# Kernel tuning notes

Hardware: AMD Instinct MI355X
Metric: run time of the kernel (lower is better)

The kernel has to match this reference:

```python
import jax, jax.numpy as jnp
import numpy as np

B, O, H2, L, S = 256, 1024, 2048, 2, 12  # batch, output_dim, 2*hidden_dim, num_layers, enc seq len


def setup_inputs() -> dict:
    key = jax.random.key(0)
    ks = jax.random.split(key, 18)
    def rn(k, shape, scale=1.0):
        return jax.random.normal(k, shape, jnp.float32) * scale
    s = 0.02  # weight scale to keep softmax/gates in a sane range
    return {
        "x": rn(ks[0], (1, B, O)),
        "h0": rn(ks[1], (L, B, H2)),
        "c0": rn(ks[2], (L, B, H2)),
        "encoder_outputs": rn(ks[3], (S, B, H2)),
        "attn_W": rn(ks[4], (S, H2 + O), s), "attn_b": rn(ks[5], (S,), s),
        "comb_W": rn(ks[6], (O, H2 + O), s), "comb_b": rn(ks[7], (O,), s),
        "Wih0": rn(ks[8], (4 * H2, O), s), "Whh0": rn(ks[9], (4 * H2, H2), s),
        "bih0": rn(ks[10], (4 * H2,), s), "bhh0": rn(ks[11], (4 * H2,), s),
        "Wih1": rn(ks[12], (4 * H2, H2), s), "Whh1": rn(ks[13], (4 * H2, H2), s),
        "bih1": rn(ks[14], (4 * H2,), s), "bhh1": rn(ks[15], (4 * H2,), s),
        "out_W": rn(ks[16], (O, H2), s), "out_b": rn(ks[17], (O,), s),
    }


def _lstm_cell(x, h, c, Wih, Whh, bih, bhh):
    # PyTorch LSTM cell: gates in (i, f, g, o) order
    gates = x @ Wih.T + bih + h @ Whh.T + bhh  # [B, 4*H2]
    i, f, g, o = jnp.split(gates, 4, axis=-1)
    c_new = jax.nn.sigmoid(f) * c + jax.nn.sigmoid(i) * jnp.tanh(g)
    h_new = jax.nn.sigmoid(o) * jnp.tanh(c_new)
    return h_new, c_new


def reference(x, h0, c0, encoder_outputs, attn_W, attn_b, comb_W, comb_b,
              Wih0, Whh0, bih0, bhh0, Wih1, Whh1, bih1, bhh1, out_W, out_b):
    x0 = x[0]  # [B, O]
    # Bahdanau-style attention over the 12 encoder steps
    attn_in = jnp.concatenate([x0, h0[0]], axis=1)               # [B, O+2H]
    attn_weights = jax.nn.softmax(attn_in @ attn_W.T + attn_b, axis=1)  # [B, S]
    attn_applied = jnp.einsum('bs,sbh->bh', attn_weights, encoder_outputs)  # [B, 2H]
    # combine + relu
    xc = jnp.concatenate([x0, attn_applied], axis=1)             # [B, O+2H]
    xin = jax.nn.relu(xc @ comb_W.T + comb_b)                    # [B, O]
    # single-step 2-layer LSTM (dropout=0)
    h1, c1 = _lstm_cell(xin, h0[0], c0[0], Wih0, Whh0, bih0, bhh0)
    h2, c2 = _lstm_cell(h1, h0[1], c0[1], Wih1, Whh1, bih1, bhh1)
    output = h2[None]                                            # [1, B, 2H]
    prediction = output @ out_W.T + out_b                        # [1, B, O]
    h_new = jnp.stack([h1, h2], axis=0)
    c_new = jnp.stack([c1, c2], axis=0)
    return prediction, h_new, c_new
```

## Files before the change

### kernel.cpp

```cpp
#include <hip/hip_runtime.h>
#include <hip/hip_bf16.h>

typedef short short8 __attribute__((ext_vector_type(8)));
typedef short short4v __attribute__((ext_vector_type(4)));
typedef float floatx4 __attribute__((ext_vector_type(4)));

#define BB 256
#define OO 1024
#define HH 2048
#define SS 12
#define LSTRIDE 72

__device__ __forceinline__ __hip_bfloat16 f2b(float x) { return __float2bfloat16(x); }
__device__ __forceinline__ float sigf(float x) { return 1.0f / (1.0f + expf(-x)); }

__device__ __forceinline__ short8 cvt8v(float4 lo, float4 hi) {
    union { short8 s; __hip_bfloat16 h[8]; } u;
    u.h[0] = f2b(lo.x); u.h[1] = f2b(lo.y); u.h[2] = f2b(lo.z); u.h[3] = f2b(lo.w);
    u.h[4] = f2b(hi.x); u.h[5] = f2b(hi.y); u.h[6] = f2b(hi.z); u.h[7] = f2b(hi.w);
    return u.s;
}
__device__ __forceinline__ short4v cvt4v(float4 v) {
    union { short4v s; __hip_bfloat16 h[4]; } u;
    u.h[0] = f2b(v.x); u.h[1] = f2b(v.y); u.h[2] = f2b(v.z); u.h[3] = f2b(v.w);
    return u.s;
}

__global__ __launch_bounds__(256)
void attn_logits(const float* __restrict__ x0,
                 const float* __restrict__ h00,
                 const float* __restrict__ attn_W,
                 const float* __restrict__ attn_b,
                 float* __restrict__ wts)
{
    const int b = blockIdx.x;
    const int tid = threadIdx.x;
    const int lane = tid & 63;
    const int wave = tid >> 6;

    float part[SS];
#pragma unroll
    for (int s = 0; s < SS; s++) part[s] = 0.f;

#pragma unroll
    for (int k = 0; k < 3; k++) {
        const int c = tid + (k << 8);
        float4 v = (k == 0) ? *(const float4*)(x0 + (size_t)b * OO + (c << 2))
                            : *(const float4*)(h00 + (size_t)b * HH + ((c - 256) << 2));
#pragma unroll
        for (int s = 0; s < SS; s++) {
            float4 w4 = *(const float4*)(attn_W + (size_t)s * (OO + HH) + (c << 2));
            part[s] += v.x * w4.x + v.y * w4.y + v.z * w4.z + v.w * w4.w;
        }
    }
#pragma unroll
    for (int s = 0; s < SS; s++) {
#pragma unroll
        for (int off = 32; off > 0; off >>= 1)
            part[s] += __shfl_down(part[s], off);
    }
    __shared__ float red[4][SS];
    if (lane == 0) {
#pragma unroll
        for (int s = 0; s < SS; s++) red[wave][s] = part[s];
    }
    __syncthreads();
    if (tid == 0) {
        float logits[SS];
        float mx = -1e30f;
        for (int s = 0; s < SS; s++) {
            logits[s] = red[0][s] + red[1][s] + red[2][s] + red[3][s] + attn_b[s];
            mx = fmaxf(mx, logits[s]);
        }
        float sum = 0.f;
        for (int s = 0; s < SS; s++) { logits[s] = expf(logits[s] - mx); sum += logits[s]; }
        float inv = 1.0f / sum;
        for (int s = 0; s < SS; s++) wts[b * SS + s] = logits[s] * inv;
    }
}

__global__ __launch_bounds__(256)
void attn_apply(const float* __restrict__ enc,
                const float* __restrict__ wts,
                float* __restrict__ attn_out)
{
    const int b = blockIdx.x >> 1;
    const int half = blockIdx.x & 1;
    const int tid = threadIdx.x;
    __shared__ float w[SS];
    if (tid < SS) w[tid] = wts[b * SS + tid];
    __syncthreads();
    const int h = (half << 10) + (tid << 2);
    float4 a = {0.f, 0.f, 0.f, 0.f};
#pragma unroll
    for (int s = 0; s < SS; s++) {
        float4 e = *(const float4*)(enc + ((size_t)(s * BB + b) * HH) + h);
        float ws = w[s];
        a.x += ws * e.x; a.y += ws * e.y; a.z += ws * e.z; a.w += ws * e.w;
    }
    *(float4*)(attn_out + (size_t)b * HH + h) = a;
}

template<int K1, int K2, bool RELU>
__global__ __launch_bounds__(256)
void gemm_dual(const float* __restrict__ A1,
               const float* __restrict__ W1, int ldw1, int ofs1,
               const float* __restrict__ A2,
               const float* __restrict__ W2, int ldw2, int ofs2,
               const float* __restrict__ bias1,
               const float* __restrict__ bias2,
               float* __restrict__ Cout, int ldc)
{
    constexpr int n1 = K1 >> 6;
    constexpr int nT = (K1 + K2) >> 6;
    __shared__ __attribute__((aligned(16))) __hip_bfloat16 As[2][16][LSTRIDE];
    __shared__ __attribute__((aligned(16))) __hip_bfloat16 Ws[2][32][LSTRIDE];
    __shared__ float red[2][16][17];
    const int tid = threadIdx.x;
    const int lane = tid & 63;
    const int wave = tid >> 6;
    const int quad = lane >> 4, l15 = lane & 15;
    const int cf = wave & 1;
    const int kh = wave >> 1;
    const int m_base = blockIdx.y * 16;
    const int n_base = blockIdx.x * 32;

    const int arow = tid >> 4, acol = (tid & 15) << 2;
    const int wrow = tid >> 3, wcol = (tid & 7) << 3;

    const float* baseA1 = A1 + (size_t)(m_base + arow) * K1 + acol;
    const float* baseA2 = A2 + (size_t)(m_base + arow) * K2 + acol;
    const float* baseW1 = W1 + (size_t)(n_base + wrow) * ldw1 + ofs1 + wcol;
    const float* baseW2 = W2 + (size_t)(n_base + wrow) * ldw2 + ofs2 + wcol;

    float4 pa, pw0, pw1;
    auto issue = [&](int tt) {
        const float *ap, *wp;
        if (tt < n1) { ap = baseA1 + (tt << 6);        wp = baseW1 + (tt << 6); }
        else         { ap = baseA2 + ((tt - n1) << 6); wp = baseW2 + ((tt - n1) << 6); }
        pa  = *(const float4*)(ap);
        pw0 = *(const float4*)(wp);
        pw1 = *(const float4*)(wp + 4);
    };
    issue(0);

    floatx4 acc = (floatx4){0.f, 0.f, 0.f, 0.f};
    for (int t = 0; t < nT; t++) {
        const int buf = t & 1;
        *(short4v*)(&As[buf][arow][acol]) = cvt4v(pa);
        *(short8*)(&Ws[buf][wrow][wcol])  = cvt8v(pw0, pw1);
        __syncthreads();
        if (t + 1 < nT) issue(t + 1);
        short8 af = *(const short8*)(&As[buf][l15][kh * 32 + quad * 8]);
        short8 bf = *(const short8*)(&Ws[buf][cf * 16 + l15][kh * 32 + quad * 8]);
        acc = __builtin_amdgcn_mfma_f32_16x16x32_bf16(af, bf, acc, 0, 0, 0);
    }

    if (kh == 1) {
#pragma unroll
        for (int r = 0; r < 4; r++) red[cf][l15][quad * 4 + r] = acc[r];
    }
    __syncthreads();
    if (kh == 0) {
        const int col = n_base + cf * 16 + l15;
        float bsum = bias1[col] + (bias2 ? bias2[col] : 0.f);
#pragma unroll
        for (int r = 0; r < 4; r++) {
            const int row = m_base + quad * 4 + r;
            float v = acc[r] + red[cf][l15][quad * 4 + r] + bsum;
            if (RELU) v = fmaxf(v, 0.f);
            Cout[(size_t)row * ldc + col] = v;
        }
    }
}

template<int K1>
__global__ __launch_bounds__(512)
void lstm_fused(const float* __restrict__ A1,
                const float* __restrict__ Wih,
                const float* __restrict__ A2,
                const float* __restrict__ Whh,
                const float* __restrict__ bih,
                const float* __restrict__ bhh,
                const float* __restrict__ c0,
                float* __restrict__ h_out,
                float* __restrict__ c_out)
{
    constexpr int n1 = K1 >> 6;
    constexpr int nT = n1 + (HH >> 6);
    __shared__ __attribute__((aligned(16))) __hip_bfloat16 As[2][128][LSTRIDE];
    __shared__ __attribute__((aligned(16))) __hip_bfloat16 Ws[2][64][LSTRIDE];
    const int tid = threadIdx.x;
    const int lane = tid & 63;
    const int wave = tid >> 6;
    const int quad = lane >> 4, l15 = lane & 15;

    const int L    = blockIdx.x + (blockIdx.y << 7);
    const int xcd  = L & 7;
    const int slot = L >> 3;
    const int by   = xcd >> 2;
    const int bx   = ((xcd & 3) << 5) + slot;
    const int m_base = by * 128;
    const int n_base = bx * 16;

    const int arow = tid >> 2, acol = (tid & 3) << 4;
    const int wrow = tid >> 3, wcol = (tid & 7) << 3;
    const int grow = (wrow >> 4) * HH + n_base + (wrow & 15);

    const float* baseA1 = A1 + (size_t)(m_base + arow) * K1 + acol;
    const float* baseA2 = A2 + (size_t)(m_base + arow) * HH + acol;
    const float* baseW1 = Wih + (size_t)grow * K1 + wcol;
    const float* baseW2 = Whh + (size_t)grow * HH + wcol;

    float4 paA[4], pwA[2], paB[4], pwB[2];
    auto issue = [&](int tt, float4 (&pa)[4], float4 (&pw)[2]) {
        const float *ap, *wp;
        if (tt < n1) { ap = baseA1 + (tt << 6);        wp = baseW1 + (tt << 6); }
        else         { ap = baseA2 + ((tt - n1) << 6); wp = baseW2 + ((tt - n1) << 6); }
#pragma unroll
        for (int j = 0; j < 4; j++) pa[j] = *(const float4*)(ap + (j << 2));
#pragma unroll
        for (int j = 0; j < 2; j++) pw[j] = *(const float4*)(wp + (j << 2));
    };
    issue(0, paA, pwA);
    issue(1, paB, pwB);

    floatx4 acc[4];
#pragma unroll
    for (int g = 0; g < 4; g++) acc[g] = (floatx4){0.f, 0.f, 0.f, 0.f};

    auto compute = [&](int buf) {
#pragma unroll
        for (int k = 0; k < 2; k++) {
            short8 af = *(const short8*)(&As[buf][wave * 16 + l15][k * 32 + quad * 8]);
#pragma unroll
            for (int g = 0; g < 4; g++) {
                short8 bf = *(const short8*)(&Ws[buf][g * 16 + l15][k * 32 + quad * 8]);
                acc[g] = __builtin_amdgcn_mfma_f32_16x16x32_bf16(af, bf, acc[g], 0, 0, 0);
            }
        }
    };

    for (int t = 0; t < nT; t += 2) {
        *(short8*)(&As[0][arow][acol])     = cvt8v(paA[0], paA[1]);
        *(short8*)(&As[0][arow][acol + 8]) = cvt8v(paA[2], paA[3]);
        *(short8*)(&Ws[0][wrow][wcol])     = cvt8v(pwA[0], pwA[1]);
        if (t + 2 < nT) issue(t + 2, paA, pwA);
        __syncthreads();
        compute(0);
        *(short8*)(&As[1][arow][acol])     = cvt8v(paB[0], paB[1]);
        *(short8*)(&As[1][arow][acol + 8]) = cvt8v(paB[2], paB[3]);
        *(short8*)(&Ws[1][wrow][wcol])     = cvt8v(pwB[0], pwB[1]);
        if (t + 3 < nT) issue(t + 3, paB, pwB);
        __syncthreads();
        compute(1);
    }

    const int col = n_base + l15;
    float bsum[4];
#pragma unroll
    for (int g = 0; g < 4; g++)
        bsum[g] = bih[g * HH + col] + bhh[g * HH + col];

#pragma unroll
    for (int r = 0; r < 4; r++) {
        const int row = m_base + wave * 16 + quad * 4 + r;
        const size_t idx = (size_t)row * HH + col;
        float gi = acc[0][r] + bsum[0];
        float gf = acc[1][r] + bsum[1];
        float gg = acc[2][r] + bsum[2];
        float go = acc[3][r] + bsum[3];
        float c0v = c0[idx];
        float cn = sigf(gf) * c0v + sigf(gi) * tanhf(gg);
        float hn = sigf(go) * tanhf(cn);
        h_out[idx] = hn;
        c_out[idx] = cn;
    }
}

extern "C" void kernel_launch(void* const* d_in, const int* in_sizes, int n_in,
                              void* d_out, int out_size, void* d_ws, size_t ws_size,
                              hipStream_t stream) {
    const float* x      = (const float*)d_in[0];
    const float* h0     = (const float*)d_in[1];
    const float* c0     = (const float*)d_in[2];
    const float* enc    = (const float*)d_in[3];
    const float* attn_W = (const float*)d_in[4];
    const float* attn_b = (const float*)d_in[5];
    const float* comb_W = (const float*)d_in[6];
    const float* comb_b = (const float*)d_in[7];
    const float* Wih0   = (const float*)d_in[8];
    const float* Whh0   = (const float*)d_in[9];
    const float* bih0   = (const float*)d_in[10];
    const float* bhh0   = (const float*)d_in[11];
    const float* Wih1   = (const float*)d_in[12];
    const float* Whh1   = (const float*)d_in[13];
    const float* bih1   = (const float*)d_in[14];
    const float* bhh1   = (const float*)d_in[15];
    const float* out_W  = (const float*)d_in[16];
    const float* out_b  = (const float*)d_in[17];

    float* pred = (float*)d_out;
    float* h1   = pred + 262144;
    float* h2   = h1 + 524288;
    float* c1   = h2 + 524288;
    float* c2   = c1 + 524288;
    const float* h0_l0 = h0;
    const float* h0_l1 = h0 + 524288;
    const float* c0_l0 = c0;
    const float* c0_l1 = c0 + 524288;

    float* xin      = pred;
    float* attn_out = c2;
    float* wts      = c1;

    attn_logits<<<dim3(BB), dim3(256), 0, stream>>>(x, h0_l0, attn_W, attn_b, wts);

    attn_apply<<<dim3(BB * 2), dim3(256), 0, stream>>>(enc, wts, attn_out);

    gemm_dual<OO, HH, true><<<dim3(OO / 32, BB / 16), dim3(256), 0, stream>>>(
        x, comb_W, OO + HH, 0,
        attn_out, comb_W, OO + HH, OO,
        comb_b, nullptr, xin, OO);

    lstm_fused<OO><<<dim3(HH / 16, BB / 128), dim3(512), 0, stream>>>(
        xin, Wih0, h0_l0, Whh0, bih0, bhh0, c0_l0, h1, c1);

    lstm_fused<HH><<<dim3(HH / 16, BB / 128), dim3(512), 0, stream>>>(
        h1, Wih1, h0_l1, Whh1, bih1, bhh1, c0_l1, h2, c2);

    gemm_dual<HH, 0, false><<<dim3(OO / 32, BB / 16), dim3(256), 0, stream>>>(
        h2, out_W, HH, 0,
        h2, out_W, HH, 0,
        out_b, nullptr, pred, OO);
}
```

Measured before the change: 404.7 us.

## Split LSTM gate GEMM into split-K tiles with swizzled LDS and separate cell kernel

Replaces the fused LSTM kernel with a split-K gate GEMM: each block covers all 256 batch rows and 32 columns per gate, with K split four ways, and writes fp32 partial gate sums to workspace. A separate elementwise kernel adds the partials and biases, then applies the LSTM cell. Larger tiles reuse each weight load across the whole batch instead of reloading it for two row halves, and XOR-swizzled LDS replaces padded rows to avoid bank conflicts. The cost is an extra launch per layer and roughly 32MB of partial-sum traffic per layer through workspace.

```diff
diff --git a/kernel.cpp b/kernel.cpp
--- a/kernel.cpp
+++ b/kernel.cpp
@@ -174,49 +174,58 @@
     }
 }
 
+#define A_BUF_BYTES 16384
+#define W_BUF_BYTES 8192
+__device__ __forceinline__ int swzA(int buf, int row, int c8) {
+    return (buf << 14) + ((((row << 6) | (c8 << 4))) ^ ((row & 7) << 4));
+}
+__device__ __forceinline__ int swzW(int buf, int row, int c8) {
+    return 2 * A_BUF_BYTES + (buf << 13) + ((((row << 6) | (c8 << 4))) ^ ((row & 7) << 4));
+}
+
 template<int K1>
 __global__ __launch_bounds__(512)
-void lstm_fused(const float* __restrict__ A1,
+void lstm_gates(const float* __restrict__ A1,
                 const float* __restrict__ Wih,
                 const float* __restrict__ A2,
                 const float* __restrict__ Whh,
-                const float* __restrict__ bih,
-                const float* __restrict__ bhh,
-                const float* __restrict__ c0,
-                float* __restrict__ h_out,
-                float* __restrict__ c_out)
-{
-    constexpr int n1 = K1 >> 6;
-    constexpr int nT = n1 + (HH >> 6);
-    __shared__ __attribute__((aligned(16))) __hip_bfloat16 As[2][128][LSTRIDE];
-    __shared__ __attribute__((aligned(16))) __hip_bfloat16 Ws[2][64][LSTRIDE];
+                float* __restrict__ P)
+{
+    constexpr int KTOT = K1 + HH;
+    constexpr int KPER = KTOT / 4;
+    constexpr int NT = KPER / 32;
+    __shared__ __attribute__((aligned(128))) unsigned char lds[2 * A_BUF_BYTES + 2 * W_BUF_BYTES];
+
     const int tid = threadIdx.x;
     const int lane = tid & 63;
     const int wave = tid >> 6;
     const int quad = lane >> 4, l15 = lane & 15;
 
-    const int L    = blockIdx.x + (blockIdx.y << 7);
+    const int L    = blockIdx.x + (blockIdx.y << 6);
     const int xcd  = L & 7;
     const int slot = L >> 3;
-    const int by   = xcd >> 2;
-    const int bx   = ((xcd & 3) << 5) + slot;
-    const int m_base = by * 128;
-    const int n_base = bx * 16;
-
-    const int arow = tid >> 2, acol = (tid & 3) << 4;
-    const int wrow = tid >> 3, wcol = (tid & 7) << 3;
-    const int grow = (wrow >> 4) * HH + n_base + (wrow & 15);
-
-    const float* baseA1 = A1 + (size_t)(m_base + arow) * K1 + acol;
-    const float* baseA2 = A2 + (size_t)(m_base + arow) * HH + acol;
-    const float* baseW1 = Wih + (size_t)grow * K1 + wcol;
-    const float* baseW2 = Whh + (size_t)grow * HH + wcol;
+    const int ks   = xcd >> 1;
+    const int nb   = ((xcd & 1) << 5) | slot;
+    const int n_base = nb << 5;
+    const int k0 = ks * KPER;
+
+    const int arow = tid >> 1;
+    const int ac8  = (tid & 1) << 1;
+    const int wrow = tid >> 2;
+    const int wc8  = tid & 3;
+    const int grow = (wrow >> 5) * HH + n_base + (wrow & 31);
+
+    const float* bA1 = A1 + (size_t)arow * K1 + (ac8 << 3);
+    const float* bA2 = A2 + (size_t)arow * HH + (ac8 << 3);
+    const float* bW1 = Wih + (size_t)grow * K1 + (wc8 << 3);
+    const float* bW2 = Whh + (size_t)grow * HH + (wc8 << 3);
 
     float4 paA[4], pwA[2], paB[4], pwB[2];
     auto issue = [&](int tt, float4 (&pa)[4], float4 (&pw)[2]) {
+        const int gk = k0 + (tt << 5);
         const float *ap, *wp;
-        if (tt < n1) { ap = baseA1 + (tt << 6);        wp = baseW1 + (tt << 6); }
-        else         { ap = baseA2 + ((tt - n1) << 6); wp = baseW2 + ((tt - n1) << 6); }
+        if (gk < K1) { ap = bA1 + gk;        wp = bW1 + gk; }
+        else         { ap = bA2 + (gk - K1); wp = bW2 + (gk - K1); }
 #pragma unroll
         for (int j = 0; j < 4; j++) pa[j] = *(const float4*)(ap + (j << 2));
 #pragma unroll
@@ -225,57 +234,104 @@
     issue(0, paA, pwA);
     issue(1, paB, pwB);
 
-    floatx4 acc[4];
-#pragma unroll
-    for (int g = 0; g < 4; g++) acc[g] = (floatx4){0.f, 0.f, 0.f, 0.f};
-
+    floatx4 acc[2][4][2];
+#pragma unroll
+    for (int mf = 0; mf < 2; mf++)
+#pragma unroll
+        for (int g = 0; g < 4; g++)
+#pragma unroll
+            for (int nf = 0; nf < 2; nf++)
+                acc[mf][g][nf] = (floatx4){0.f, 0.f, 0.f, 0.f};
+
+    auto store_tile = [&](int buf, float4 (&pa)[4], float4 (&pw)[2]) {
+        *(short8*)(lds + swzA(buf, arow, ac8))     = cvt8v(pa[0], pa[1]);
+        *(short8*)(lds + swzA(buf, arow, ac8 | 1)) = cvt8v(pa[2], pa[3]);
+        *(short8*)(lds + swzW(buf, wrow, wc8))     = cvt8v(pw[0], pw[1]);
+    };
     auto compute = [&](int buf) {
-#pragma unroll
-        for (int k = 0; k < 2; k++) {
-            short8 af = *(const short8*)(&As[buf][wave * 16 + l15][k * 32 + quad * 8]);
-#pragma unroll
-            for (int g = 0; g < 4; g++) {
-                short8 bf = *(const short8*)(&Ws[buf][g * 16 + l15][k * 32 + quad * 8]);
-                acc[g] = __builtin_amdgcn_mfma_f32_16x16x32_bf16(af, bf, acc[g], 0, 0, 0);
+        short8 af[2];
+#pragma unroll
+        for (int mf = 0; mf < 2; mf++)
+            af[mf] = *(const short8*)(lds + swzA(buf, (wave << 5) + (mf << 4) + l15, quad));
+#pragma unroll
+        for (int g = 0; g < 4; g++)
+#pragma unroll
+            for (int nf = 0; nf < 2; nf++) {
+                short8 bf = *(const short8*)(lds + swzW(buf, (g << 5) + (nf << 4) + l15, quad));
+                acc[0][g][nf] = __builtin_amdgcn_mfma_f32_16x16x32_bf16(af[0], bf, acc[0][g][nf], 0, 0, 0);
+                acc[1][g][nf] = __builtin_amdgcn_mfma_f32_16x16x32_bf16(af[1], bf, acc[1][g][nf], 0, 0, 0);
             }
-        }
     };
 
-    for (int t = 0; t < nT; t += 2) {
-        *(short8*)(&As[0][arow][acol])     = cvt8v(paA[0], paA[1]);
-        *(short8*)(&As[0][arow][acol + 8]) = cvt8v(paA[2], paA[3]);
-        *(short8*)(&Ws[0][wrow][wcol])     = cvt8v(pwA[0], pwA[1]);
-        if (t + 2 < nT) issue(t + 2, paA, pwA);
+    for (int t = 0; t < NT; t += 2) {
+        store_tile(0, paA, pwA);
+        if (t + 2 < NT) issue(t + 2, paA, pwA);
         __syncthreads();
         compute(0);
-        *(short8*)(&As[1][arow][acol])     = cvt8v(paB[0], paB[1]);
-        *(short8*)(&As[1][arow][acol + 8]) = cvt8v(paB[2], paB[3]);
-        *(short8*)(&Ws[1][wrow][wcol])     = cvt8v(pwB[0], pwB[1]);
-        if (t + 3 < nT) issue(t + 3, paB, pwB);
+        store_tile(1, paB, pwB);
+        if (t + 3 < NT) issue(t + 3, paB, pwB);
         __syncthreads();
         compute(1);
     }
 
-    const int col = n_base + l15;
-    float bsum[4];
-#pragma unroll
-    for (int g = 0; g < 4; g++)
-        bsum[g] = bih[g * HH + col] + bhh[g * HH + col];
-
-#pragma unroll
-    for (int r = 0; r < 4; r++) {
-        const int row = m_base + wave * 16 + quad * 4 + r;
-        const size_t idx = (size_t)row * HH + col;
-        float gi = acc[0][r] + bsum[0];
-        float gf = acc[1][r] + bsum[1];
-        float gg = acc[2][r] + bsum[2];
-        float go = acc[3][r] + bsum[3];
-        float c0v = c0[idx];
-        float cn = sigf(gf) * c0v + sigf(gi) * tanhf(gg);
-        float hn = sigf(go) * tanhf(cn);
-        h_out[idx] = hn;
-        c_out[idx] = cn;
-    }
+    float* Pk = P + (size_t)ks * (256 * 8192);
+#pragma unroll
+    for (int mf = 0; mf < 2; mf++)
+#pragma unroll
+        for (int g = 0; g < 4; g++)
+#pragma unroll
+            for (int nf = 0; nf < 2; nf++) {
+                const int col = n_base + (nf << 4) + l15;
+#pragma unroll
+                for (int r = 0; r < 4; r++) {
+                    const int row = (wave << 5) + (mf << 4) + (quad << 2) + r;
+                    Pk[(size_t)row * 8192 + g * HH + col] = acc[mf][g][nf][r];
+                }
+            }
+}
+
+__global__ __launch_bounds__(512)
+void lstm_cell(const float* __restrict__ P,
+               const float* __restrict__ bih,
+               const float* __restrict__ bhh,
+               const float* __restrict__ c0,
+               float* __restrict__ h_out,
+               float* __restrict__ c_out)
+{
+    const int gid = blockIdx.x * 512 + threadIdx.x;
+    const int row = gid >> 9;
+    const int col = (gid & 511) << 2;
+
+    float4 gate[4];
+#pragma unroll
+    for (int g = 0; g < 4; g++) {
+        const size_t base = (size_t)row * 8192 + g * HH + col;
+        float4 s = *(const float4*)(P + base);
+#pragma unroll
+        for (int k = 1; k < 4; k++) {
+            float4 v = *(const float4*)(P + (size_t)k * (256 * 8192) + base);
+            s.x += v.x; s.y += v.y; s.z += v.z; s.w += v.w;
+        }
+        float4 b1 = *(const float4*)(bih + g * HH + col);
+        float4 b2 = *(const float4*)(bhh + g * HH + col);
+        s.x += b1.x + b2.x; s.y += b1.y + b2.y; s.z += b1.z + b2.z; s.w += b1.w + b2.w;
+        gate[g] = s;
+    }
+    const size_t idx = (size_t)row * HH + col;
+    float4 cv = *(const float4*)(c0 + idx);
+    float4 hn, cn;
+    {
+        float c_ = sigf(gate[1].x) * cv.x + sigf(gate[0].x) * tanhf(gate[2].x);
+        cn.x = c_; hn.x = sigf(gate[3].x) * tanhf(c_);
+        c_ = sigf(gate[1].y) * cv.y + sigf(gate[0].y) * tanhf(gate[2].y);
+        cn.y = c_; hn.y = sigf(gate[3].y) * tanhf(c_);
+        c_ = sigf(gate[1].z) * cv.z + sigf(gate[0].z) * tanhf(gate[2].z);
+        cn.z = c_; hn.z = sigf(gate[3].z) * tanhf(c_);
+        c_ = sigf(gate[1].w) * cv.w + sigf(gate[0].w) * tanhf(gate[2].w);
+        cn.w = c_; hn.w = sigf(gate[3].w) * tanhf(c_);
+    }
+    *(float4*)(h_out + idx) = hn;
+    *(float4*)(c_out + idx) = cn;
 }
 
 extern "C" void kernel_launch(void* const* d_in, const int* in_sizes, int n_in,
@@ -313,6 +369,7 @@
     float* xin      = pred;
     float* attn_out = c2;
     float* wts      = c1;
+    float* P        = (float*)d_ws;
 
     attn_logits<<<dim3(BB), dim3(256), 0, stream>>>(x, h0_l0, attn_W, attn_b, wts);
 
@@ -323,11 +380,11 @@
         attn_out, comb_W, OO + HH, OO,
         comb_b, nullptr, xin, OO);
 
-    lstm_fused<OO><<<dim3(HH / 16, BB / 128), dim3(512), 0, stream>>>(
-        xin, Wih0, h0_l0, Whh0, bih0, bhh0, c0_l0, h1, c1);
-
-    lstm_fused<HH><<<dim3(HH / 16, BB / 128), dim3(512), 0, stream>>>(
-        h1, Wih1, h0_l1, Whh1, bih1, bhh1, c0_l1, h2, c2);
+    lstm_gates<OO><<<dim3(64, 4), dim3(512), 0, stream>>>(xin, Wih0, h0_l0, Whh0, P);
+    lstm_cell<<<dim3(256), dim3(512), 0, stream>>>(P, bih0, bhh0, c0_l0, h1, c1);
+
+    lstm_gates<HH><<<dim3(64, 4), dim3(512), 0, stream>>>(h1, Wih1, h0_l1, Whh1, P);
+    lstm_cell<<<dim3(256), dim3(512), 0, stream>>>(P, bih1, bhh1, c0_l1, h2, c2);
 
     gemm_dual<HH, 0, false><<<dim3(OO / 32, BB / 16), dim3(256), 0, stream>>>(
         h2, out_W, HH, 0,
```

Result: no change. 398.8 us (-1.4%).
